# Kernel optimization log

Hardware: AMD Instinct MI355X
Metric: run time of the kernel (lower is better)

The kernel has to match this reference:

```python
import jax, jax.numpy as jnp
import numpy as np

N = 2097152   # number of points
TDIM = 16     # t_feat dim
HID = 64      # map_st hidden
BIG = 10000.0 # outer-bin extension from get_xy_compute


def setup_inputs() -> dict:
    key = jax.random.key(0)
    ks = jax.random.split(key, 4)
    x = jax.random.normal(ks[0], (N, 3), dtype=jnp.float32)
    t_feat = jax.random.normal(ks[1], (N, TDIM), dtype=jnp.float32)
    mask = jnp.array([1.0, 1.0, 0.0], dtype=jnp.float32)
    W1 = jax.random.normal(ks[2], (2 + TDIM, HID), dtype=jnp.float32) * 0.1
    b1 = jnp.zeros((HID,), dtype=jnp.float32)
    W2 = jax.random.normal(ks[3], (HID, 10), dtype=jnp.float32) * 0.1
    b2 = jnp.zeros((10,), dtype=jnp.float32)
    return {"x": x, "t_feat": t_feat, "mask": mask,
            "W1": W1, "b1": b1, "W2": W2, "b2": b2}


def _map_st(a, t, W1, b1, W2, b2):
    # a: [N,2] tanh of masked channels; t: [N,TDIM] -> [N,10] positive params
    z = jnp.concatenate([a, t], axis=-1)
    h = jax.nn.relu(z @ W1 + b1)
    return jax.nn.softplus(h @ W2 + b2) + 1e-4


def _get_xy(d):
    # d: [N,10] = dxl2,dxl1,dxr1,dxr2,dyl2,dyl1,dyr1,dyr2,kl,kr  (split order in get_all_xy)
    dxl2, dxl1, dxr1, dxr2 = d[..., 0], d[..., 1], d[..., 2], d[..., 3]
    dyl2, dyl1, dyr1, dyr2 = d[..., 4], d[..., 5], d[..., 6], d[..., 7]
    kl, kr = d[..., 8] * 2.0, d[..., 9] * 2.0
    xL1 = -dxl1;            yL1 = -dyl1
    xL2 = -dxl1 - dxl2;     yL2 = -dyl1 - dyl2
    xR1 = dxr1;             yR1 = dyr1
    xR2 = dxr1 + dxr2;      yR2 = dyr1 + dyr2
    xR3 = xR2 + BIG;        yR3 = yR2 + kr * BIG
    xL3 = xL2 - BIG;        yL3 = yL2 - kl * BIG
    all_x = jnp.stack([xL3, xL2, xL1, xR1, xR2, xR3], axis=-1)  # [N,6] monotonic
    all_y = jnp.stack([yL3, yL2, yL1, yR1, yR2, yR3], axis=-1)
    return all_x, all_y


def _interp(xk, yk, qx):
    # xk,yk: [N,6] knots; qx: [N]. Piecewise-linear interpolation (InterpGrad.forw_compute out).
    xl, xr = xk[..., :-1], xk[..., 1:]
    yl, yr = yk[..., :-1], yk[..., 1:]
    qx = jnp.clip(qx, xl[..., 0] * 0.99, xr[..., -1] * 0.99)
    q = qx[..., None]                       # [N,1]
    in_range = (q >= xl) & (q < xr)         # exactly one bin per row after clamp
    vals = (yr - yl) / (xr - xl) * (q - xl) + yl
    return jnp.sum(jnp.where(in_range, vals, 0.0), axis=-1)


def reference(x, t_feat, mask, W1, b1, W2, b2):
    # mask = [1,1,0]: channels 0,1 condition; channel 2 is transformed
    y_base = x * mask
    a = jnp.tanh(x[..., :2])
    d = _map_st(a, t_feat, W1, b1, W2, b2)
    all_x, all_y = _get_xy(d)
    out = _interp(all_x, all_y, x[..., 2])  # [N]
    return jnp.concatenate([y_base[..., :2], out[..., None]], axis=-1)
```

## Files before the change

### kernel.cpp

```cpp
#include <hip/hip_runtime.h>
#include <hip/hip_bf16.h>

typedef __attribute__((ext_vector_type(8))) short bf16x8;
typedef __attribute__((ext_vector_type(4))) float f32x4;
typedef __attribute__((ext_vector_type(4))) int   i32x4;

#define BIGC 10000.0f
#define TPW 4
#define WAVES 4

__device__ __forceinline__ float fast_exp2(float x) { return __builtin_amdgcn_exp2f(x); }
__device__ __forceinline__ float fast_log2(float x) { return __builtin_amdgcn_logf(x); }
__device__ __forceinline__ float fast_rcp(float x)  { return __builtin_amdgcn_rcpf(x); }

__device__ __forceinline__ float fast_tanh(float x) {
    const float ax = fabsf(x);
    const float e  = fast_exp2(ax * 2.8853900817779268f);
    const float r  = 1.0f - 2.0f * fast_rcp(e + 1.0f);
    return copysignf(r, x);
}
__device__ __forceinline__ float fast_softplus(float v) {
    const float e = fast_exp2(fabsf(v) * -1.4426950408889634f);
    const float l = fast_log2(1.0f + e) * 0.6931471805599453f;
    return fmaxf(v, 0.0f) + l;
}
__device__ __forceinline__ unsigned pack2bf(float hi, float lo) {
    unsigned r;
    asm("v_cvt_pk_bf16_f32 %0, %1, %2" : "=v"(r) : "v"(lo), "v"(hi));
    return r;
}

__global__ void __launch_bounds__(256, 4) coupling_mfma4(
    const float* __restrict__ x, const float* __restrict__ t_feat,
    const float* __restrict__ mask, const float* __restrict__ W1,
    const float* __restrict__ b1, const float* __restrict__ W2,
    const float* __restrict__ b2, float* __restrict__ out, int n)
{
    __shared__ float lds_d[WAVES][64][11];

    const int wave = threadIdx.x >> 6;
    const int lane = threadIdx.x & 63;
    const int m    = lane & 15;
    const int q    = lane >> 4;
    const int m4   = m << 2;

    bf16x8 w1f[4];
#pragma unroll
    for (int a = 0; a < 4; ++a) {
        float wv[8];
#pragma unroll
        for (int j = 0; j < 8; ++j) {
            const int k = q * 8 + j;
            const int col = 16 * a + m;
            float v = 0.0f;
            if (k < 16)       v = W1[(k + 2) * 64 + col];
            else if (k == 16) v = W1[0 * 64 + col];
            else if (k == 17) v = W1[1 * 64 + col];
            else if (k == 18) v = b1[col];
            wv[j] = v;
        }
        i32x4 f = { (int)pack2bf(wv[1], wv[0]), (int)pack2bf(wv[3], wv[2]),
                    (int)pack2bf(wv[5], wv[4]), (int)pack2bf(wv[7], wv[6]) };
        w1f[a] = __builtin_bit_cast(bf16x8, f);
    }
    bf16x8 w2f[2];
#pragma unroll
    for (int fi = 0; fi < 2; ++fi) {
        float wv[8];
#pragma unroll
        for (int j = 0; j < 8; ++j) {
            const int hid = 32 * fi + 16 * (j >> 2) + 4 * q + (j & 3);
            wv[j] = (m < 10) ? W2[hid * 10 + m] : 0.0f;
        }
        i32x4 f = { (int)pack2bf(wv[1], wv[0]), (int)pack2bf(wv[3], wv[2]),
                    (int)pack2bf(wv[5], wv[4]), (int)pack2bf(wv[7], wv[6]) };
        w2f[fi] = __builtin_bit_cast(bf16x8, f);
    }
    const float bias2 = (m < 10) ? b2[m] : 0.0f;
    const float m0 = mask[0], m1 = mask[1];

    for (int it = 0; it < TPW; ++it) {
        int pb = (blockIdx.x * TPW + it) * (WAVES * 64) + wave * 64;
        pb = min(pb, n - 64);
        pb = max(pb, 0);

        const int pl  = pb + lane;
        const int plc = min(pl, n - 1);
        const float* xp = x + plc * 3;
        const float xi0 = xp[0], xi1 = xp[1], xi2 = xp[2];

        float4 ta[4], tb[4];
        if (q < 2) {
#pragma unroll
            for (int s = 0; s < 4; ++s) {
                const int ps = min(pb + 16 * s + m, n - 1);
                const float4* tr = (const float4*)(t_feat + ps * 16 + q * 8);
                ta[s] = tr[0];
                tb[s] = tr[1];
            }
        }

        const unsigned pk = pack2bf(fast_tanh(xi1), fast_tanh(xi0));

#pragma unroll
        for (int s = 0; s < 4; ++s) {
            const int tp = __builtin_amdgcn_ds_bpermute(s * 64 + m4, (int)pk);

            i32x4 zw = { 0, 0, 0, 0 };
            if (q < 2) {
                zw[0] = (int)pack2bf(ta[s].y, ta[s].x);
                zw[1] = (int)pack2bf(ta[s].w, ta[s].z);
                zw[2] = (int)pack2bf(tb[s].y, tb[s].x);
                zw[3] = (int)pack2bf(tb[s].w, tb[s].z);
            } else if (q == 2) {
                zw[0] = tp;
                zw[1] = 0x3F80;
            }
            const bf16x8 zf = __builtin_bit_cast(bf16x8, zw);

            f32x4 acc[4];
#pragma unroll
            for (int a = 0; a < 4; ++a) {
                f32x4 c = { 0.0f, 0.0f, 0.0f, 0.0f };
                acc[a] = __builtin_amdgcn_mfma_f32_16x16x32_bf16(w1f[a], zf, c, 0, 0, 0);
            }

            float rl[16];
#pragma unroll
            for (int a = 0; a < 4; ++a)
#pragma unroll
                for (int r = 0; r < 4; ++r)
                    rl[4 * a + r] = fmaxf(acc[a][r], 0.0f);
            i32x4 a20 = { (int)pack2bf(rl[1],  rl[0]),  (int)pack2bf(rl[3],  rl[2]),
                          (int)pack2bf(rl[5],  rl[4]),  (int)pack2bf(rl[7],  rl[6]) };
            i32x4 a21 = { (int)pack2bf(rl[9],  rl[8]),  (int)pack2bf(rl[11], rl[10]),
                          (int)pack2bf(rl[13], rl[12]), (int)pack2bf(rl[15], rl[14]) };

            f32x4 cb = { bias2, bias2, bias2, bias2 };
            f32x4 cz = { 0.0f, 0.0f, 0.0f, 0.0f };
            f32x4 cd0 = __builtin_amdgcn_mfma_f32_16x16x32_bf16(
                            __builtin_bit_cast(bf16x8, a20), w2f[0], cb, 0, 0, 0);
            f32x4 cd1 = __builtin_amdgcn_mfma_f32_16x16x32_bf16(
                            __builtin_bit_cast(bf16x8, a21), w2f[1], cz, 0, 0, 0);

#pragma unroll
            for (int r = 0; r < 4; ++r) {
                const float dv = fast_softplus(cd0[r] + cd1[r]) + 0.0001f;
                if (m < 10) lds_d[wave][16 * s + 4 * q + r][m] = dv;
            }
        }

        {
            const float* dd = lds_d[wave][lane];
            const float dxl2 = dd[0], dxl1 = dd[1], dxr1 = dd[2], dxr2 = dd[3];
            const float dyl2 = dd[4], dyl1 = dd[5], dyr1 = dd[6], dyr2 = dd[7];
            const float kl = dd[8] * 2.0f, kr = dd[9] * 2.0f;

            const float xL1 = -dxl1,        yL1 = -dyl1;
            const float xL2 = -dxl1 - dxl2, yL2 = -dyl1 - dyl2;
            const float xR1 = dxr1,         yR1 = dyr1;
            const float xR2 = dxr1 + dxr2,  yR2 = dyr1 + dyr2;
            const float xR3 = xR2 + BIGC,   yR3 = fmaf(kr, BIGC, yR2);
            const float xL3 = xL2 - BIGC,   yL3 = fmaf(-kl, BIGC, yL2);

            float qx = fminf(fmaxf(xi2, xL3 * 0.99f), xR3 * 0.99f);
            float xl = xL3, xrr = xL2, yl = yL3, yr = yL2;
            if (qx >= xL2) { xl = xL2; xrr = xL1; yl = yL2; yr = yL1; }
            if (qx >= xL1) { xl = xL1; xrr = xR1; yl = yL1; yr = yR1; }
            if (qx >= xR1) { xl = xR1; xrr = xR2; yl = yR1; yr = yR2; }
            if (qx >= xR2) { xl = xR2; xrr = xR3; yl = yR2; yr = yR3; }
            const float slope = (yr - yl) * fast_rcp(xrr - xl);
            const float res = fmaf(slope, qx - xl, yl);

            if (pl < n) {
                float* op = out + pl * 3;
                op[0] = xi0 * m0;
                op[1] = xi1 * m1;
                op[2] = res;
            }
        }
    }
}

extern "C" void kernel_launch(void* const* d_in, const int* in_sizes, int n_in,
                              void* d_out, int out_size, void* d_ws, size_t ws_size,
                              hipStream_t stream) {
    const float* x      = (const float*)d_in[0];
    const float* t_feat = (const float*)d_in[1];
    const float* mask   = (const float*)d_in[2];
    const float* W1     = (const float*)d_in[3];
    const float* b1     = (const float*)d_in[4];
    const float* W2     = (const float*)d_in[5];
    const float* b2     = (const float*)d_in[6];
    float* out = (float*)d_out;

    const int n = in_sizes[0] / 3;
    const int pts_per_block = TPW * WAVES * 64;
    const int grid = (n + pts_per_block - 1) / pts_per_block;
    coupling_mfma4<<<grid, 256, 0, stream>>>(x, t_feat, mask, W1, b1, W2, b2, out, n);
}
```

Before: 235.6 us.

## Software-pipeline input loads and batch MFMAs across four sub-tiles

Loads the x and t_feat values for the next iteration before the current iteration's MFMA chain runs, so global-memory latency overlaps with compute. It also restructures the inner loop so all 16 first-layer MFMAs and all 8 second-layer MFMAs are issued back-to-back, which exposes independent matrix ops to the scheduler. Launch bounds drop from 4 to 3 waves per SIMD to make room for the extra registers. It also removes the n-1 clamps and the pl<n store guard, which assumes n is a multiple of 64, and the lower occupancy cuts how much latency other waves can hide.

```diff
diff --git a/kernel.cpp b/kernel.cpp
--- a/kernel.cpp
+++ b/kernel.cpp
@@ -30,7 +30,7 @@
     return r;
 }
 
-__global__ void __launch_bounds__(256, 4) coupling_mfma4(
+__global__ void __launch_bounds__(256, 3) coupling_mfma5(
     const float* __restrict__ x, const float* __restrict__ t_feat,
     const float* __restrict__ mask, const float* __restrict__ W1,
     const float* __restrict__ b1, const float* __restrict__ W2,
@@ -79,76 +79,112 @@
     const float bias2 = (m < 10) ? b2[m] : 0.0f;
     const float m0 = mask[0], m1 = mask[1];
 
+    const int pbase = blockIdx.x * (TPW * WAVES * 64) + wave * 64;
+
+    float4 tA[4], tB[4];
+    float xi0, xi1, xi2;
+    {
+        const int pb = max(min(pbase, n - 64), 0);
+        const float* xp = x + (pb + lane) * 3;
+        xi0 = xp[0]; xi1 = xp[1]; xi2 = xp[2];
+        if (q < 2) {
+#pragma unroll
+            for (int s = 0; s < 4; ++s) {
+                const float4* tr = (const float4*)(t_feat + (pb + 16 * s + m) * 16 + q * 8);
+                tA[s] = tr[0]; tB[s] = tr[1];
+            }
+        }
+    }
+
+#pragma unroll
     for (int it = 0; it < TPW; ++it) {
-        int pb = (blockIdx.x * TPW + it) * (WAVES * 64) + wave * 64;
-        pb = min(pb, n - 64);
-        pb = max(pb, 0);
-
-        const int pl  = pb + lane;
-        const int plc = min(pl, n - 1);
-        const float* xp = x + plc * 3;
-        const float xi0 = xp[0], xi1 = xp[1], xi2 = xp[2];
-
-        float4 ta[4], tb[4];
-        if (q < 2) {
-#pragma unroll
-            for (int s = 0; s < 4; ++s) {
-                const int ps = min(pb + 16 * s + m, n - 1);
-                const float4* tr = (const float4*)(t_feat + ps * 16 + q * 8);
-                ta[s] = tr[0];
-                tb[s] = tr[1];
-            }
-        }
-
-        const unsigned pk = pack2bf(fast_tanh(xi1), fast_tanh(xi0));
-
-#pragma unroll
-        for (int s = 0; s < 4; ++s) {
-            const int tp = __builtin_amdgcn_ds_bpermute(s * 64 + m4, (int)pk);
-
-            i32x4 zw = { 0, 0, 0, 0 };
+        const int pb = max(min(pbase + it * (WAVES * 64), n - 64), 0);
+
+        const float sx0 = xi0, sx1 = xi1, sx2 = xi2;
+
+        const unsigned pk = pack2bf(fast_tanh(sx1), fast_tanh(sx0));
+
+        int tp[4];
+#pragma unroll
+        for (int s = 0; s < 4; ++s)
+            tp[s] = __builtin_amdgcn_ds_bpermute(s * 64 + m4, (int)pk);
+
+        i32x4 zw[4];
+#pragma unroll
+        for (int s = 0; s < 4; ++s) {
+            zw[s][0] = 0; zw[s][1] = 0; zw[s][2] = 0; zw[s][3] = 0;
             if (q < 2) {
-                zw[0] = (int)pack2bf(ta[s].y, ta[s].x);
-                zw[1] = (int)pack2bf(ta[s].w, ta[s].z);
-                zw[2] = (int)pack2bf(tb[s].y, tb[s].x);
-                zw[3] = (int)pack2bf(tb[s].w, tb[s].z);
+                zw[s][0] = (int)pack2bf(tA[s].y, tA[s].x);
+                zw[s][1] = (int)pack2bf(tA[s].w, tA[s].z);
+                zw[s][2] = (int)pack2bf(tB[s].y, tB[s].x);
+                zw[s][3] = (int)pack2bf(tB[s].w, tB[s].z);
             } else if (q == 2) {
-                zw[0] = tp;
-                zw[1] = 0x3F80;
-            }
-            const bf16x8 zf = __builtin_bit_cast(bf16x8, zw);
-
-            f32x4 acc[4];
+                zw[s][0] = tp[s];
+                zw[s][1] = 0x3F80;
+            }
+        }
+
+        if (it + 1 < TPW) {
+            const int pb2 = max(min(pbase + (it + 1) * (WAVES * 64), n - 64), 0);
+            const float* xp = x + (pb2 + lane) * 3;
+            xi0 = xp[0]; xi1 = xp[1]; xi2 = xp[2];
+            if (q < 2) {
+#pragma unroll
+                for (int s = 0; s < 4; ++s) {
+                    const float4* tr = (const float4*)(t_feat + (pb2 + 16 * s + m) * 16 + q * 8);
+                    tA[s] = tr[0]; tB[s] = tr[1];
+                }
+            }
+        }
+
+        f32x4 acc[4][4];
+#pragma unroll
+        for (int s = 0; s < 4; ++s) {
+            const bf16x8 zf = __builtin_bit_cast(bf16x8, zw[s]);
 #pragma unroll
             for (int a = 0; a < 4; ++a) {
                 f32x4 c = { 0.0f, 0.0f, 0.0f, 0.0f };
-                acc[a] = __builtin_amdgcn_mfma_f32_16x16x32_bf16(w1f[a], zf, c, 0, 0, 0);
-            }
-
+                acc[s][a] = __builtin_amdgcn_mfma_f32_16x16x32_bf16(w1f[a], zf, c, 0, 0, 0);
+            }
+        }
+
+        i32x4 a20[4], a21[4];
+#pragma unroll
+        for (int s = 0; s < 4; ++s) {
             float rl[16];
 #pragma unroll
             for (int a = 0; a < 4; ++a)
 #pragma unroll
                 for (int r = 0; r < 4; ++r)
-                    rl[4 * a + r] = fmaxf(acc[a][r], 0.0f);
-            i32x4 a20 = { (int)pack2bf(rl[1],  rl[0]),  (int)pack2bf(rl[3],  rl[2]),
-                          (int)pack2bf(rl[5],  rl[4]),  (int)pack2bf(rl[7],  rl[6]) };
-            i32x4 a21 = { (int)pack2bf(rl[9],  rl[8]),  (int)pack2bf(rl[11], rl[10]),
-                          (int)pack2bf(rl[13], rl[12]), (int)pack2bf(rl[15], rl[14]) };
-
-            f32x4 cb = { bias2, bias2, bias2, bias2 };
-            f32x4 cz = { 0.0f, 0.0f, 0.0f, 0.0f };
-            f32x4 cd0 = __builtin_amdgcn_mfma_f32_16x16x32_bf16(
-                            __builtin_bit_cast(bf16x8, a20), w2f[0], cb, 0, 0, 0);
-            f32x4 cd1 = __builtin_amdgcn_mfma_f32_16x16x32_bf16(
-                            __builtin_bit_cast(bf16x8, a21), w2f[1], cz, 0, 0, 0);
-
+                    rl[4 * a + r] = fmaxf(acc[s][a][r], 0.0f);
+            a20[s][0] = (int)pack2bf(rl[1],  rl[0]);
+            a20[s][1] = (int)pack2bf(rl[3],  rl[2]);
+            a20[s][2] = (int)pack2bf(rl[5],  rl[4]);
+            a20[s][3] = (int)pack2bf(rl[7],  rl[6]);
+            a21[s][0] = (int)pack2bf(rl[9],  rl[8]);
+            a21[s][1] = (int)pack2bf(rl[11], rl[10]);
+            a21[s][2] = (int)pack2bf(rl[13], rl[12]);
+            a21[s][3] = (int)pack2bf(rl[15], rl[14]);
+        }
+
+        f32x4 cd0[4], cd1[4];
+        const f32x4 cb = { bias2, bias2, bias2, bias2 };
+        const f32x4 cz = { 0.0f, 0.0f, 0.0f, 0.0f };
+#pragma unroll
+        for (int s = 0; s < 4; ++s) {
+            cd0[s] = __builtin_amdgcn_mfma_f32_16x16x32_bf16(
+                         __builtin_bit_cast(bf16x8, a20[s]), w2f[0], cb, 0, 0, 0);
+            cd1[s] = __builtin_amdgcn_mfma_f32_16x16x32_bf16(
+                         __builtin_bit_cast(bf16x8, a21[s]), w2f[1], cz, 0, 0, 0);
+        }
+
+#pragma unroll
+        for (int s = 0; s < 4; ++s)
 #pragma unroll
             for (int r = 0; r < 4; ++r) {
-                const float dv = fast_softplus(cd0[r] + cd1[r]) + 0.0001f;
+                const float dv = fast_softplus(cd0[s][r] + cd1[s][r]) + 0.0001f;
                 if (m < 10) lds_d[wave][16 * s + 4 * q + r][m] = dv;
             }
-        }
 
         {
             const float* dd = lds_d[wave][lane];
@@ -163,7 +199,7 @@
             const float xR3 = xR2 + BIGC,   yR3 = fmaf(kr, BIGC, yR2);
             const float xL3 = xL2 - BIGC,   yL3 = fmaf(-kl, BIGC, yL2);
 
-            float qx = fminf(fmaxf(xi2, xL3 * 0.99f), xR3 * 0.99f);
+            float qx = fminf(fmaxf(sx2, xL3 * 0.99f), xR3 * 0.99f);
             float xl = xL3, xrr = xL2, yl = yL3, yr = yL2;
             if (qx >= xL2) { xl = xL2; xrr = xL1; yl = yL2; yr = yL1; }
             if (qx >= xL1) { xl = xL1; xrr = xR1; yl = yL1; yr = yR1; }
@@ -172,12 +208,10 @@
             const float slope = (yr - yl) * fast_rcp(xrr - xl);
             const float res = fmaf(slope, qx - xl, yl);
 
-            if (pl < n) {
-                float* op = out + pl * 3;
-                op[0] = xi0 * m0;
-                op[1] = xi1 * m1;
-                op[2] = res;
-            }
+            float* op = out + (pb + lane) * 3;
+            op[0] = sx0 * m0;
+            op[1] = sx1 * m1;
+            op[2] = res;
         }
     }
 }
@@ -197,5 +231,5 @@
     const int n = in_sizes[0] / 3;
     const int pts_per_block = TPW * WAVES * 64;
     const int grid = (n + pts_per_block - 1) / pts_per_block;
-    coupling_mfma4<<<grid, 256, 0, stream>>>(x, t_feat, mask, W1, b1, W2, b2, out, n);
-}
+    coupling_mfma5<<<grid, 256, 0, stream>>>(x, t_feat, mask, W1, b1, W2, b2, out, n);
+}
```

Result: no change. 235.3 us (-0.1%).
